# Performance work log

Hardware: AMD Instinct MI355X
Metric: run time of the kernel (lower is better)

Reference implementation:

```python
import jax, jax.numpy as jnp
import numpy as np

# Approximate EMD matching (Fan et al. approxmatch): 10 annealed soft-assignment
# rounds with levels -4^j for j = 7..-1 and level 0 for the final round.
_LEVELS = jnp.asarray([-(4.0 ** j) for j in range(7, -2, -1)] + [0.0], dtype=jnp.float32)


def _approx_match(d2, n, m):
    # d2: [b, n, m] squared pairwise distances
    b = d2.shape[0]
    factorl = max(n, m) / float(n)
    factorr = max(n, m) / float(m)
    remainl0 = jnp.full((b, n), factorl, dtype=d2.dtype)
    remainr0 = jnp.full((b, m), factorr, dtype=d2.dtype)
    match0 = jnp.zeros_like(d2)

    def step(carry, level):
        match, remainl, remainr = carry
        w = jnp.exp(level * d2) * remainr[:, None, :]            # [b,n,m]
        w = w / (jnp.sum(w, axis=-1, keepdims=True) + 1e-9)      # row-normalize
        w = w * remainl[:, :, None]                              # scale by left capacity
        ss2 = jnp.sum(w, axis=1)                                 # [b,m] column mass
        s = jnp.minimum(remainr / (ss2 + 1e-9), 1.0)             # column saturation
        w = w * s[:, None, :]
        match = match + w
        remainl = jnp.maximum(remainl - jnp.sum(w, axis=-1), 0.0)
        remainr = jnp.maximum(remainr - jnp.sum(w, axis=1), 0.0)
        return (match, remainl, remainr), None

    (match, _, _), _ = jax.lax.scan(step, (match0, remainl0, remainr0), _LEVELS)
    return match


def setup_inputs() -> dict:
    key = jax.random.key(0)
    k1, k2 = jax.random.split(key)
    xyz1 = jax.random.normal(k1, (16, 2048, 3), dtype=jnp.float32)
    xyz2 = jax.random.normal(k2, (16, 2048, 3), dtype=jnp.float32)
    return {"xyz1": xyz1, "xyz2": xyz2}


def reference(xyz1, xyz2):
    n, m = xyz1.shape[1], xyz2.shape[1]
    diff = xyz1[:, :, None, :] - xyz2[:, None, :, :]             # [b,n,m,3]
    d2 = jnp.sum(diff * diff, axis=-1)                           # [b,n,m]
    match = _approx_match(d2, n, m)
    dist = jnp.sqrt(jnp.maximum(d2, 1e-12))
    cost = jnp.sum(match * dist, axis=(1, 2))                    # [b]
    return cost
```

## Files before the change

### kernel.cpp

```cpp
#include <hip/hip_runtime.h>
#include <math.h>

#define B 16
#define N 2048
#define M 2048
#define BN (B * N)
#define LOG2E 1.4426950408889634f

#define CJ 128
#define NCH (M / CJ)
#define TPB 128
#define RPT 4
#define RBLK (TPB * RPT)

#define EXP2F(x) __builtin_amdgcn_exp2f(x)
#define SQRTF(x) __builtin_amdgcn_sqrtf(x)

__global__ __launch_bounds__(1024) void k_sort(const float* __restrict__ xyz1,
                                               const float* __restrict__ xyz2,
                                               float4* __restrict__ p1,
                                               float4* __restrict__ p2,
                                               float2* __restrict__ ib,
                                               float2* __restrict__ jb) {
    __shared__ float key[2048];
    __shared__ int sidx[2048];
    const int wg = blockIdx.x;
    const int b = wg & (B - 1);
    const bool second = wg >= B;
    const float* src = second ? xyz2 : xyz1;
    const int tx = threadIdx.x;

    for (int t = tx; t < 2048; t += 1024) {
        key[t] = src[3 * (size_t)(b * 2048 + t)];
        sidx[t] = t;
    }
    __syncthreads();

    for (int k = 2; k <= 2048; k <<= 1) {
        for (int j = k >> 1; j > 0; j >>= 1) {
            int e = 2 * tx - (tx & (j - 1));
            int f = e + j;
            bool asc = ((e & k) == 0);
            float ke = key[e], kf = key[f];
            if ((ke > kf) == asc) {
                int ie = sidx[e], if_ = sidx[f];
                key[e] = kf;
                key[f] = ke;
                sidx[e] = if_;
                sidx[f] = ie;
            }
            __syncthreads();
        }
    }

    float4* dst = second ? p2 : p1;
    for (int t = tx; t < 2048; t += 1024) {
        int o = sidx[t];
        const float* s = src + 3 * (size_t)(b * 2048 + o);
        float x = s[0], y = s[1], z = s[2];
        dst[b * 2048 + t] = make_float4(x, y, z, fmaf(x, x, fmaf(y, y, z * z)));
    }
    if (tx < NCH) {
        float2 bb = make_float2(key[tx * CJ], key[tx * CJ + CJ - 1]);
        (second ? jb : ib)[b * NCH + tx] = bb;
    }
}

__global__ __launch_bounds__(256) void k_init(float* __restrict__ rl0,
                                              float* __restrict__ rr0,
                                              float* __restrict__ rs0,
                                              float* __restrict__ rs2,
                                              float* __restrict__ t1b,
                                              float* __restrict__ ss20,
                                              float* __restrict__ cost) {
    int idx = blockIdx.x * 256 + threadIdx.x;
    rl0[idx] = 1.0f;
    rr0[idx] = 1.0f;
    rs0[idx] = 0.0f;
    rs2[idx] = 0.0f;
    t1b[idx] = 0.0f;
    ss20[idx] = 0.0f;
    if (idx < B) cost[idx] = 0.0f;
}

__global__ __launch_bounds__(TPB, 2) void k_rowsum0(const float4* __restrict__ p1,
                                                    const float4* __restrict__ p2,
                                                    const float2* __restrict__ jb,
                                                    float* __restrict__ rs,
                                                    float c2, float sqD) {
    __shared__ float4 tile4[CJ];
    const int b = blockIdx.z;
    const int tx = threadIdx.x;
    const int i0 = blockIdx.y * RBLK + 4 * tx;

    {
        int gj = b * M + blockIdx.x * CJ + tx;
        float4 f = p2[gj];
        tile4[tx] = make_float4(f.x, f.y, f.z, c2 * f.w);
    }
    __syncthreads();

    float4 f0 = p1[b * N + i0];
    float4 f1 = p1[b * N + i0 + 1];
    float4 f2 = p1[b * N + i0 + 2];
    float4 f3 = p1[b * N + i0 + 3];
    float2 bnd = jb[b * NCH + blockIdx.x];
    bool skip = (bnd.x - f3.x > sqD) || (f0.x - bnd.y > sqD);

    float a0 = 0.0f, a1 = 0.0f, a2 = 0.0f, a3 = 0.0f;
    if (!skip) {
        const float m2c = -2.0f * c2;
        float X0 = m2c * f0.x, Y0 = m2c * f0.y, Z0 = m2c * f0.z, n0 = c2 * f0.w;
        float X1 = m2c * f1.x, Y1 = m2c * f1.y, Z1 = m2c * f1.z, n1 = c2 * f1.w;
        float X2 = m2c * f2.x, Y2 = m2c * f2.y, Z2 = m2c * f2.z, n2 = c2 * f2.w;
        float X3 = m2c * f3.x, Y3 = m2c * f3.y, Z3 = m2c * f3.z, n3 = c2 * f3.w;
#pragma unroll 8
        for (int t = 0; t < CJ; ++t) {
            float4 q4 = tile4[t];
            a0 += EXP2F(fmaf(q4.x, X0, fmaf(q4.y, Y0, fmaf(q4.z, Z0, n0 + q4.w))));
            a1 += EXP2F(fmaf(q4.x, X1, fmaf(q4.y, Y1, fmaf(q4.z, Z1, n1 + q4.w))));
            a2 += EXP2F(fmaf(q4.x, X2, fmaf(q4.y, Y2, fmaf(q4.z, Z2, n2 + q4.w))));
            a3 += EXP2F(fmaf(q4.x, X3, fmaf(q4.y, Y3, fmaf(q4.z, Z3, n3 + q4.w))));
        }
    }
    atomicAdd(&rs[b * N + i0], a0);
    atomicAdd(&rs[b * N + i0 + 1], a1);
    atomicAdd(&rs[b * N + i0 + 2], a2);
    atomicAdd(&rs[b * N + i0 + 3], a3);
}

__global__ __launch_bounds__(TPB, 2) void k_colsum(const float4* __restrict__ p1,
                                                   const float4* __restrict__ p2,
                                                   const float2* __restrict__ ib,
                                                   const float* __restrict__ rl_in,
                                                   float* __restrict__ rl_out,
                                                   const float* __restrict__ rs_prev,
                                                   const float* __restrict__ rs_cur,
                                                   float* __restrict__ rs_zero,
                                                   const float* __restrict__ t1_in,
                                                   float* __restrict__ t1_zero,
                                                   const float* __restrict__ rr,
                                                   float* __restrict__ ss2_acc,
                                                   float cS, float sqD) {
    __shared__ float4 tile4[CJ];
    __shared__ float tileA[CJ];
    const int b = blockIdx.z;
    const int tx = threadIdx.x;
    const int j0 = blockIdx.y * RBLK + 4 * tx;

    {
        int gi = b * N + blockIdx.x * CJ + tx;
        float4 f = p1[gi];
        float rlo = rl_in[gi];
        float ap = rlo / (rs_prev[gi] + 1e-9f);
        float rln = fmaxf(rlo - ap * t1_in[gi], 0.0f);
        float a = rln / (rs_cur[gi] + 1e-9f);
        tile4[tx] = make_float4(f.x, f.y, f.z, cS * f.w);
        tileA[tx] = a;
        if (blockIdx.y == 0) {
            rl_out[gi] = rln;
            t1_zero[gi] = 0.0f;
            rs_zero[gi] = 0.0f;
        }
    }
    __syncthreads();

    float4 f0 = p2[b * M + j0];
    float4 f1 = p2[b * M + j0 + 1];
    float4 f2 = p2[b * M + j0 + 2];
    float4 f3 = p2[b * M + j0 + 3];
    float2 bnd = ib[b * NCH + blockIdx.x];
    bool skip = (bnd.x - f3.x > sqD) || (f0.x - bnd.y > sqD);

    float a0 = 0.0f, a1 = 0.0f, a2 = 0.0f, a3 = 0.0f;
    if (!skip) {
        const float m2c = -2.0f * cS;
        float X0 = m2c * f0.x, Y0 = m2c * f0.y, Z0 = m2c * f0.z, n0 = cS * f0.w;
        float X1 = m2c * f1.x, Y1 = m2c * f1.y, Z1 = m2c * f1.z, n1 = cS * f1.w;
        float X2 = m2c * f2.x, Y2 = m2c * f2.y, Z2 = m2c * f2.z, n2 = cS * f2.w;
        float X3 = m2c * f3.x, Y3 = m2c * f3.y, Z3 = m2c * f3.z, n3 = cS * f3.w;
#pragma unroll 8
        for (int t = 0; t < CJ; ++t) {
            float4 q4 = tile4[t];
            float av = tileA[t];
            a0 = fmaf(EXP2F(fmaf(q4.x, X0, fmaf(q4.y, Y0, fmaf(q4.z, Z0, n0 + q4.w)))), av, a0);
            a1 = fmaf(EXP2F(fmaf(q4.x, X1, fmaf(q4.y, Y1, fmaf(q4.z, Z1, n1 + q4.w)))), av, a1);
            a2 = fmaf(EXP2F(fmaf(q4.x, X2, fmaf(q4.y, Y2, fmaf(q4.z, Z2, n2 + q4.w)))), av, a2);
            a3 = fmaf(EXP2F(fmaf(q4.x, X3, fmaf(q4.y, Y3, fmaf(q4.z, Z3, n3 + q4.w)))), av, a3);
        }
    }
    atomicAdd(&ss2_acc[b * M + j0], a0 * rr[b * M + j0]);
    atomicAdd(&ss2_acc[b * M + j0 + 1], a1 * rr[b * M + j0 + 1]);
    atomicAdd(&ss2_acc[b * M + j0 + 2], a2 * rr[b * M + j0 + 2]);
    atomicAdd(&ss2_acc[b * M + j0 + 3], a3 * rr[b * M + j0 + 3]);
}

__global__ __launch_bounds__(256) void k_suma(const float* __restrict__ rl_in,
                                              float* __restrict__ rl_out,
                                              const float* __restrict__ rs_prev,
                                              const float* __restrict__ rs_cur,
                                              const float* __restrict__ t1_in,
                                              float* __restrict__ S) {
    __shared__ float red[4];
    const int b = blockIdx.x;
    const int tx = threadIdx.x;
    float s = 0.0f;
#pragma unroll
    for (int k = 0; k < N / 256; ++k) {
        int gi = b * N + k * 256 + tx;
        float rlo = rl_in[gi];
        float ap = rlo / (rs_prev[gi] + 1e-9f);
        float rln = fmaxf(rlo - ap * t1_in[gi], 0.0f);
        rl_out[gi] = rln;
        s += rln / (rs_cur[gi] + 1e-9f);
    }
#pragma unroll
    for (int off = 32; off > 0; off >>= 1)
        s += __shfl_down(s, off, 64);
    if ((tx & 63) == 0) red[tx >> 6] = s;
    __syncthreads();
    if (tx == 0) S[b] = red[0] + red[1] + red[2] + red[3];
}

__global__ __launch_bounds__(256) void k_mulss2(const float* __restrict__ rr,
                                                const float* __restrict__ S,
                                                float* __restrict__ ss2_out) {
    int idx = blockIdx.x * 256 + threadIdx.x;
    ss2_out[idx] = rr[idx] * S[idx >> 11];
}

template <int MODE>
__global__ __launch_bounds__(TPB, 2) void k_fused(const float4* __restrict__ p1,
                                                  const float4* __restrict__ p2,
                                                  const float2* __restrict__ jb,
                                                  const float* __restrict__ rr_in,
                                                  float* __restrict__ rr_out,
                                                  const float* __restrict__ ss2_in,
                                                  float* __restrict__ ss2_zero,
                                                  const float* __restrict__ rl_new,
                                                  const float* __restrict__ rs_cur,
                                                  float* __restrict__ rs_next,
                                                  float* __restrict__ t1_acc,
                                                  float* __restrict__ cost,
                                                  float cS, float rsq, float sqD) {
    __shared__ float4 tile4[CJ];
    __shared__ float2 tile2[CJ];
    const int b = blockIdx.z;
    const int tx = threadIdx.x;
    const int i0 = blockIdx.y * RBLK + 4 * tx;

    {
        int gj = b * M + blockIdx.x * CJ + tx;
        float4 f = p2[gj];
        float rrv = rr_in[gj];
        float sv = ss2_in[gj];
        float s = fminf(rrv / (sv + 1e-9f), 1.0f);
        float q = rrv * s;
        float rrn = fmaxf(rrv - sv * s, 0.0f);
        tile4[tx] = make_float4(f.x, f.y, f.z, q);
        tile2[tx] = make_float2(rrn, cS * f.w);
        if (MODE != 2 && blockIdx.y == 0) {
            rr_out[gj] = rrn;
            ss2_zero[gj] = 0.0f;
        }
    }
    __syncthreads();

    float4 f0 = p1[b * N + i0];
    float4 f1 = p1[b * N + i0 + 1];
    float4 f2 = p1[b * N + i0 + 2];
    float4 f3 = p1[b * N + i0 + 3];
    float2 bnd = jb[b * NCH + blockIdx.x];
    bool skip = (MODE == 0) && ((bnd.x - f3.x > sqD) || (f0.x - bnd.y > sqD));

    float T10 = 0.0f, T11 = 0.0f, T12 = 0.0f, T13 = 0.0f;
    float T20 = 0.0f, T21 = 0.0f, T22 = 0.0f, T23 = 0.0f;
    float rs0 = 0.0f, rs1 = 0.0f, rs2v = 0.0f, rs3 = 0.0f;
    if (!skip) {
        const float m2c = -2.0f * cS;
        float X0 = m2c * f0.x, Y0 = m2c * f0.y, Z0 = m2c * f0.z, n0 = cS * f0.w;
        float X1 = m2c * f1.x, Y1 = m2c * f1.y, Z1 = m2c * f1.z, n1 = cS * f1.w;
        float X2 = m2c * f2.x, Y2 = m2c * f2.y, Z2 = m2c * f2.z, n2 = cS * f2.w;
        float X3 = m2c * f3.x, Y3 = m2c * f3.y, Z3 = m2c * f3.z, n3 = cS * f3.w;
#pragma unroll 8
        for (int t = 0; t < CJ; ++t) {
            float4 q4 = tile4[t];
            float2 rn = tile2[t];
            float g0 = fmaf(q4.x, X0, fmaf(q4.y, Y0, fmaf(q4.z, Z0, n0 + rn.y)));
            float g1 = fmaf(q4.x, X1, fmaf(q4.y, Y1, fmaf(q4.z, Z1, n1 + rn.y)));
            float g2 = fmaf(q4.x, X2, fmaf(q4.y, Y2, fmaf(q4.z, Z2, n2 + rn.y)));
            float g3 = fmaf(q4.x, X3, fmaf(q4.y, Y3, fmaf(q4.z, Z3, n3 + rn.y)));
            float sd0 = SQRTF(fabsf(g0)), sd1 = SQRTF(fabsf(g1));
            float sd2 = SQRTF(fabsf(g2)), sd3 = SQRTF(fabsf(g3));
            float w0, w1, w2, w3;
            if (MODE == 0) {
                float e0 = EXP2F(g0), e1 = EXP2F(g1), e2 = EXP2F(g2), e3 = EXP2F(g3);
                float s0 = e0 * e0, s1 = e1 * e1, s2 = e2 * e2, s3 = e3 * e3;
                w0 = (s0 * s0) * q4.w;
                w1 = (s1 * s1) * q4.w;
                w2 = (s2 * s2) * q4.w;
                w3 = (s3 * s3) * q4.w;
                rs0 = fmaf(e0, rn.x, rs0);
                rs1 = fmaf(e1, rn.x, rs1);
                rs2v = fmaf(e2, rn.x, rs2v);
                rs3 = fmaf(e3, rn.x, rs3);
            } else if (MODE == 1) {
                w0 = EXP2F(g0) * q4.w;
                w1 = EXP2F(g1) * q4.w;
                w2 = EXP2F(g2) * q4.w;
                w3 = EXP2F(g3) * q4.w;
                rs0 += rn.x;
                rs1 += rn.x;
                rs2v += rn.x;
                rs3 += rn.x;
            } else {
                w0 = q4.w;
                w1 = q4.w;
                w2 = q4.w;
                w3 = q4.w;
            }
            T10 += w0;
            T11 += w1;
            T12 += w2;
            T13 += w3;
            T20 = fmaf(w0, sd0, T20);
            T21 = fmaf(w1, sd1, T21);
            T22 = fmaf(w2, sd2, T22);
            T23 = fmaf(w3, sd3, T23);
        }
    }

    const int gi0 = b * N + i0;
    if (MODE != 2) {
        atomicAdd(&t1_acc[gi0], T10);
        atomicAdd(&t1_acc[gi0 + 1], T11);
        atomicAdd(&t1_acc[gi0 + 2], T12);
        atomicAdd(&t1_acc[gi0 + 3], T13);
        atomicAdd(&rs_next[gi0], rs0);
        atomicAdd(&rs_next[gi0 + 1], rs1);
        atomicAdd(&rs_next[gi0 + 2], rs2v);
        atomicAdd(&rs_next[gi0 + 3], rs3);
    }

    float aa = rl_new[gi0] / (rs_cur[gi0] + 1e-9f);
    float ab = rl_new[gi0 + 1] / (rs_cur[gi0 + 1] + 1e-9f);
    float ac = rl_new[gi0 + 2] / (rs_cur[gi0 + 2] + 1e-9f);
    float ad = rl_new[gi0 + 3] / (rs_cur[gi0 + 3] + 1e-9f);
    float contrib = rsq * fmaf(aa, T20, fmaf(ab, T21, fmaf(ac, T22, ad * T23)));
#pragma unroll
    for (int off = 32; off > 0; off >>= 1)
        contrib += __shfl_down(contrib, off, 64);
    if ((tx & 63) == 0) atomicAdd(&cost[b], contrib);
}

extern "C" void kernel_launch(void* const* d_in, const int* in_sizes, int n_in,
                              void* d_out, int out_size, void* d_ws, size_t ws_size,
                              hipStream_t stream) {
    const float* xyz1 = (const float*)d_in[0];
    const float* xyz2 = (const float*)d_in[1];
    float* cost = (float*)d_out;

    float* ws = (float*)d_ws;
    float* rl[2] = {ws + 0 * BN, ws + 1 * BN};
    float* rr[2] = {ws + 2 * BN, ws + 3 * BN};
    float* rs[3] = {ws + 4 * BN, ws + 5 * BN, ws + 6 * BN};
    float* ss2b[2] = {ws + 7 * BN, ws + 8 * BN};
    float* t1[2] = {ws + 9 * BN, ws + 10 * BN};
    float4* p1 = (float4*)(ws + 11 * BN);
    float4* p2 = (float4*)(ws + 15 * BN);
    float* S = ws + 19 * BN;
    float2* ib = (float2*)(ws + 19 * BN + 64);
    float2* jb = (float2*)(ws + 19 * BN + 64 + 512);

    static const float levels[10] = {-16384.0f, -4096.0f, -1024.0f, -256.0f,
                                     -64.0f,    -16.0f,   -4.0f,    -1.0f,
                                     -0.25f,    0.0f};
    float c2[10], sqD[10];
    for (int l = 0; l < 10; ++l) {
        c2[l] = levels[l] * LOG2E;
        sqD[l] = (l < 9) ? sqrtf(150.0f / fabsf(c2[l])) : 1e30f;
    }

    dim3 grid(NCH, N / RBLK, B);
    dim3 blk(TPB);
    dim3 gs(BN / 256);
    dim3 b256(256);

    k_sort<<<dim3(2 * B), dim3(1024), 0, stream>>>(xyz1, xyz2, p1, p2, ib, jb);
    k_init<<<gs, b256, 0, stream>>>(rl[0], rr[0], rs[0], rs[2], t1[1], ss2b[0], cost);
    k_rowsum0<<<grid, blk, 0, stream>>>(p1, p2, jb, rs[0], c2[0], sqD[0]);

    for (int l = 0; l < 10; ++l) {
        int p = l & 1;
        if (l < 9) {
            k_colsum<<<grid, blk, 0, stream>>>(
                p1, p2, ib, rl[p], rl[1 - p], rs[(l + 2) % 3], rs[l % 3],
                rs[(l + 1) % 3], t1[1 - p], t1[p], rr[p], ss2b[p], c2[l], sqD[l]);
        } else {
            k_suma<<<dim3(B), b256, 0, stream>>>(
                rl[p], rl[1 - p], rs[(l + 2) % 3], rs[l % 3], t1[1 - p], S);
            k_mulss2<<<gs, b256, 0, stream>>>(rr[p], S, ss2b[p]);
        }

        if (l <= 7) {
            float cS = c2[l + 1];
            float rsq = 1.0f / sqrtf(fabsf(cS));
            k_fused<0><<<grid, blk, 0, stream>>>(
                p1, p2, jb, rr[p], rr[1 - p], ss2b[p], ss2b[1 - p], rl[1 - p],
                rs[l % 3], rs[(l + 1) % 3], t1[p], cost, cS, rsq, sqD[l + 1]);
        } else if (l == 8) {
            float cS = c2[8];
            float rsq = 1.0f / sqrtf(fabsf(cS));
            k_fused<1><<<grid, blk, 0, stream>>>(
                p1, p2, jb, rr[p], rr[1 - p], ss2b[p], ss2b[1 - p], rl[1 - p],
                rs[l % 3], rs[(l + 1) % 3], t1[p], cost, cS, rsq, 1e30f);
        } else {
            k_fused<2><<<grid, blk, 0, stream>>>(
                p1, p2, jb, rr[p], rr[1 - p], ss2b[p], ss2b[1 - p], rl[1 - p],
                rs[l % 3], rs[(l + 1) % 3], t1[p], cost, 1.0f, 1.0f, 1e30f);
        }
    }
}
```

Baseline: 669.7 us.

## Shrink blocks to one wavefront and skip whole tiles via block-level bounds

Halves the threads per block to a single 64-lane wavefront and switches each thread's four rows from a contiguous stride to a TPB stride, so global loads and atomics are coalesced. The distance-based culling test moves from a per-thread check to a per-block early return using the first and last sorted x of the block's range. Whole wavefronts can then exit before doing any exp work. The risk is more, smaller blocks, looped tile loads, and a coarser cull that may skip fewer tiles.

```diff
diff --git a/kernel.cpp b/kernel.cpp
--- a/kernel.cpp
+++ b/kernel.cpp
@@ -9,7 +9,7 @@
 
 #define CJ 128
 #define NCH (M / CJ)
-#define TPB 128
+#define TPB 64
 #define RPT 4
 #define RBLK (TPB * RPT)
 
@@ -91,42 +91,44 @@
     __shared__ float4 tile4[CJ];
     const int b = blockIdx.z;
     const int tx = threadIdx.x;
-    const int i0 = blockIdx.y * RBLK + 4 * tx;
-
-    {
-        int gj = b * M + blockIdx.x * CJ + tx;
+    const int base = blockIdx.y * RBLK;
+    const int i0 = base + tx;
+
+    for (int t = tx; t < CJ; t += TPB) {
+        int gj = b * M + blockIdx.x * CJ + t;
         float4 f = p2[gj];
-        tile4[tx] = make_float4(f.x, f.y, f.z, c2 * f.w);
+        tile4[t] = make_float4(f.x, f.y, f.z, c2 * f.w);
     }
     __syncthreads();
 
+    float2 bnd = jb[b * NCH + blockIdx.x];
+    float rlo = p1[b * N + base].x;
+    float rhi = p1[b * N + base + RBLK - 1].x;
+    if ((bnd.x - rhi > sqD) || (rlo - bnd.y > sqD)) return;
+
     float4 f0 = p1[b * N + i0];
-    float4 f1 = p1[b * N + i0 + 1];
-    float4 f2 = p1[b * N + i0 + 2];
-    float4 f3 = p1[b * N + i0 + 3];
-    float2 bnd = jb[b * NCH + blockIdx.x];
-    bool skip = (bnd.x - f3.x > sqD) || (f0.x - bnd.y > sqD);
+    float4 f1 = p1[b * N + i0 + TPB];
+    float4 f2 = p1[b * N + i0 + 2 * TPB];
+    float4 f3 = p1[b * N + i0 + 3 * TPB];
+    const float m2c = -2.0f * c2;
+    float X0 = m2c * f0.x, Y0 = m2c * f0.y, Z0 = m2c * f0.z, n0 = c2 * f0.w;
+    float X1 = m2c * f1.x, Y1 = m2c * f1.y, Z1 = m2c * f1.z, n1 = c2 * f1.w;
+    float X2 = m2c * f2.x, Y2 = m2c * f2.y, Z2 = m2c * f2.z, n2 = c2 * f2.w;
+    float X3 = m2c * f3.x, Y3 = m2c * f3.y, Z3 = m2c * f3.z, n3 = c2 * f3.w;
 
     float a0 = 0.0f, a1 = 0.0f, a2 = 0.0f, a3 = 0.0f;
-    if (!skip) {
-        const float m2c = -2.0f * c2;
-        float X0 = m2c * f0.x, Y0 = m2c * f0.y, Z0 = m2c * f0.z, n0 = c2 * f0.w;
-        float X1 = m2c * f1.x, Y1 = m2c * f1.y, Z1 = m2c * f1.z, n1 = c2 * f1.w;
-        float X2 = m2c * f2.x, Y2 = m2c * f2.y, Z2 = m2c * f2.z, n2 = c2 * f2.w;
-        float X3 = m2c * f3.x, Y3 = m2c * f3.y, Z3 = m2c * f3.z, n3 = c2 * f3.w;
 #pragma unroll 8
-        for (int t = 0; t < CJ; ++t) {
-            float4 q4 = tile4[t];
-            a0 += EXP2F(fmaf(q4.x, X0, fmaf(q4.y, Y0, fmaf(q4.z, Z0, n0 + q4.w))));
-            a1 += EXP2F(fmaf(q4.x, X1, fmaf(q4.y, Y1, fmaf(q4.z, Z1, n1 + q4.w))));
-            a2 += EXP2F(fmaf(q4.x, X2, fmaf(q4.y, Y2, fmaf(q4.z, Z2, n2 + q4.w))));
-            a3 += EXP2F(fmaf(q4.x, X3, fmaf(q4.y, Y3, fmaf(q4.z, Z3, n3 + q4.w))));
-        }
+    for (int t = 0; t < CJ; ++t) {
+        float4 q4 = tile4[t];
+        a0 += EXP2F(fmaf(q4.x, X0, fmaf(q4.y, Y0, fmaf(q4.z, Z0, n0 + q4.w))));
+        a1 += EXP2F(fmaf(q4.x, X1, fmaf(q4.y, Y1, fmaf(q4.z, Z1, n1 + q4.w))));
+        a2 += EXP2F(fmaf(q4.x, X2, fmaf(q4.y, Y2, fmaf(q4.z, Z2, n2 + q4.w))));
+        a3 += EXP2F(fmaf(q4.x, X3, fmaf(q4.y, Y3, fmaf(q4.z, Z3, n3 + q4.w))));
     }
     atomicAdd(&rs[b * N + i0], a0);
-    atomicAdd(&rs[b * N + i0 + 1], a1);
-    atomicAdd(&rs[b * N + i0 + 2], a2);
-    atomicAdd(&rs[b * N + i0 + 3], a3);
+    atomicAdd(&rs[b * N + i0 + TPB], a1);
+    atomicAdd(&rs[b * N + i0 + 2 * TPB], a2);
+    atomicAdd(&rs[b * N + i0 + 3 * TPB], a3);
 }
 
 __global__ __launch_bounds__(TPB, 2) void k_colsum(const float4* __restrict__ p1,
@@ -146,17 +148,18 @@
     __shared__ float tileA[CJ];
     const int b = blockIdx.z;
     const int tx = threadIdx.x;
-    const int j0 = blockIdx.y * RBLK + 4 * tx;
-
-    {
-        int gi = b * N + blockIdx.x * CJ + tx;
+    const int base = blockIdx.y * RBLK;
+    const int j0 = base + tx;
+
+    for (int t = tx; t < CJ; t += TPB) {
+        int gi = b * N + blockIdx.x * CJ + t;
         float4 f = p1[gi];
         float rlo = rl_in[gi];
         float ap = rlo / (rs_prev[gi] + 1e-9f);
         float rln = fmaxf(rlo - ap * t1_in[gi], 0.0f);
         float a = rln / (rs_cur[gi] + 1e-9f);
-        tile4[tx] = make_float4(f.x, f.y, f.z, cS * f.w);
-        tileA[tx] = a;
+        tile4[t] = make_float4(f.x, f.y, f.z, cS * f.w);
+        tileA[t] = a;
         if (blockIdx.y == 0) {
             rl_out[gi] = rln;
             t1_zero[gi] = 0.0f;
@@ -165,34 +168,35 @@
     }
     __syncthreads();
 
+    float2 bnd = ib[b * NCH + blockIdx.x];
+    float clo = p2[b * M + base].x;
+    float chi = p2[b * M + base + RBLK - 1].x;
+    if ((bnd.x - chi > sqD) || (clo - bnd.y > sqD)) return;
+
     float4 f0 = p2[b * M + j0];
-    float4 f1 = p2[b * M + j0 + 1];
-    float4 f2 = p2[b * M + j0 + 2];
-    float4 f3 = p2[b * M + j0 + 3];
-    float2 bnd = ib[b * NCH + blockIdx.x];
-    bool skip = (bnd.x - f3.x > sqD) || (f0.x - bnd.y > sqD);
+    float4 f1 = p2[b * M + j0 + TPB];
+    float4 f2 = p2[b * M + j0 + 2 * TPB];
+    float4 f3 = p2[b * M + j0 + 3 * TPB];
+    const float m2c = -2.0f * cS;
+    float X0 = m2c * f0.x, Y0 = m2c * f0.y, Z0 = m2c * f0.z, n0 = cS * f0.w;
+    float X1 = m2c * f1.x, Y1 = m2c * f1.y, Z1 = m2c * f1.z, n1 = cS * f1.w;
+    float X2 = m2c * f2.x, Y2 = m2c * f2.y, Z2 = m2c * f2.z, n2 = cS * f2.w;
+    float X3 = m2c * f3.x, Y3 = m2c * f3.y, Z3 = m2c * f3.z, n3 = cS * f3.w;
 
     float a0 = 0.0f, a1 = 0.0f, a2 = 0.0f, a3 = 0.0f;
-    if (!skip) {
-        const float m2c = -2.0f * cS;
-        float X0 = m2c * f0.x, Y0 = m2c * f0.y, Z0 = m2c * f0.z, n0 = cS * f0.w;
-        float X1 = m2c * f1.x, Y1 = m2c * f1.y, Z1 = m2c * f1.z, n1 = cS * f1.w;
-        float X2 = m2c * f2.x, Y2 = m2c * f2.y, Z2 = m2c * f2.z, n2 = cS * f2.w;
-        float X3 = m2c * f3.x, Y3 = m2c * f3.y, Z3 = m2c * f3.z, n3 = cS * f3.w;
 #pragma unroll 8
-        for (int t = 0; t < CJ; ++t) {
-            float4 q4 = tile4[t];
-            float av = tileA[t];
-            a0 = fmaf(EXP2F(fmaf(q4.x, X0, fmaf(q4.y, Y0, fmaf(q4.z, Z0, n0 + q4.w)))), av, a0);
-            a1 = fmaf(EXP2F(fmaf(q4.x, X1, fmaf(q4.y, Y1, fmaf(q4.z, Z1, n1 + q4.w)))), av, a1);
-            a2 = fmaf(EXP2F(fmaf(q4.x, X2, fmaf(q4.y, Y2, fmaf(q4.z, Z2, n2 + q4.w)))), av, a2);
-            a3 = fmaf(EXP2F(fmaf(q4.x, X3, fmaf(q4.y, Y3, fmaf(q4.z, Z3, n3 + q4.w)))), av, a3);
-        }
+    for (int t = 0; t < CJ; ++t) {
+        float4 q4 = tile4[t];
+        float av = tileA[t];
+        a0 = fmaf(EXP2F(fmaf(q4.x, X0, fmaf(q4.y, Y0, fmaf(q4.z, Z0, n0 + q4.w)))), av, a0);
+        a1 = fmaf(EXP2F(fmaf(q4.x, X1, fmaf(q4.y, Y1, fmaf(q4.z, Z1, n1 + q4.w)))), av, a1);
+        a2 = fmaf(EXP2F(fmaf(q4.x, X2, fmaf(q4.y, Y2, fmaf(q4.z, Z2, n2 + q4.w)))), av, a2);
+        a3 = fmaf(EXP2F(fmaf(q4.x, X3, fmaf(q4.y, Y3, fmaf(q4.z, Z3, n3 + q4.w)))), av, a3);
     }
     atomicAdd(&ss2_acc[b * M + j0], a0 * rr[b * M + j0]);
-    atomicAdd(&ss2_acc[b * M + j0 + 1], a1 * rr[b * M + j0 + 1]);
-    atomicAdd(&ss2_acc[b * M + j0 + 2], a2 * rr[b * M + j0 + 2]);
-    atomicAdd(&ss2_acc[b * M + j0 + 3], a3 * rr[b * M + j0 + 3]);
+    atomicAdd(&ss2_acc[b * M + j0 + TPB], a1 * rr[b * M + j0 + TPB]);
+    atomicAdd(&ss2_acc[b * M + j0 + 2 * TPB], a2 * rr[b * M + j0 + 2 * TPB]);
+    atomicAdd(&ss2_acc[b * M + j0 + 3 * TPB], a3 * rr[b * M + j0 + 3 * TPB]);
 }
 
 __global__ __launch_bounds__(256) void k_suma(const float* __restrict__ rl_in,
@@ -247,18 +251,19 @@
     __shared__ float2 tile2[CJ];
     const int b = blockIdx.z;
     const int tx = threadIdx.x;
-    const int i0 = blockIdx.y * RBLK + 4 * tx;
-
-    {
-        int gj = b * M + blockIdx.x * CJ + tx;
+    const int base = blockIdx.y * RBLK;
+    const int i0 = base + tx;
+
+    for (int t = tx; t < CJ; t += TPB) {
+        int gj = b * M + blockIdx.x * CJ + t;
         float4 f = p2[gj];
         float rrv = rr_in[gj];
         float sv = ss2_in[gj];
         float s = fminf(rrv / (sv + 1e-9f), 1.0f);
         float q = rrv * s;
         float rrn = fmaxf(rrv - sv * s, 0.0f);
-        tile4[tx] = make_float4(f.x, f.y, f.z, q);
-        tile2[tx] = make_float2(rrn, cS * f.w);
+        tile4[t] = make_float4(f.x, f.y, f.z, q);
+        tile2[t] = make_float2(rrn, cS * f.w);
         if (MODE != 2 && blockIdx.y == 0) {
             rr_out[gj] = rrn;
             ss2_zero[gj] = 0.0f;
@@ -266,91 +271,94 @@
     }
     __syncthreads();
 
+    if (MODE == 0) {
+        float2 bnd = jb[b * NCH + blockIdx.x];
+        float rlo = p1[b * N + base].x;
+        float rhi = p1[b * N + base + RBLK - 1].x;
+        if ((bnd.x - rhi > sqD) || (rlo - bnd.y > sqD)) return;
+    }
+
     float4 f0 = p1[b * N + i0];
-    float4 f1 = p1[b * N + i0 + 1];
-    float4 f2 = p1[b * N + i0 + 2];
-    float4 f3 = p1[b * N + i0 + 3];
-    float2 bnd = jb[b * NCH + blockIdx.x];
-    bool skip = (MODE == 0) && ((bnd.x - f3.x > sqD) || (f0.x - bnd.y > sqD));
+    float4 f1 = p1[b * N + i0 + TPB];
+    float4 f2 = p1[b * N + i0 + 2 * TPB];
+    float4 f3 = p1[b * N + i0 + 3 * TPB];
+    const float m2c = -2.0f * cS;
+    float X0 = m2c * f0.x, Y0 = m2c * f0.y, Z0 = m2c * f0.z, n0 = cS * f0.w;
+    float X1 = m2c * f1.x, Y1 = m2c * f1.y, Z1 = m2c * f1.z, n1 = cS * f1.w;
+    float X2 = m2c * f2.x, Y2 = m2c * f2.y, Z2 = m2c * f2.z, n2 = cS * f2.w;
+    float X3 = m2c * f3.x, Y3 = m2c * f3.y, Z3 = m2c * f3.z, n3 = cS * f3.w;
 
     float T10 = 0.0f, T11 = 0.0f, T12 = 0.0f, T13 = 0.0f;
     float T20 = 0.0f, T21 = 0.0f, T22 = 0.0f, T23 = 0.0f;
     float rs0 = 0.0f, rs1 = 0.0f, rs2v = 0.0f, rs3 = 0.0f;
-    if (!skip) {
-        const float m2c = -2.0f * cS;
-        float X0 = m2c * f0.x, Y0 = m2c * f0.y, Z0 = m2c * f0.z, n0 = cS * f0.w;
-        float X1 = m2c * f1.x, Y1 = m2c * f1.y, Z1 = m2c * f1.z, n1 = cS * f1.w;
-        float X2 = m2c * f2.x, Y2 = m2c * f2.y, Z2 = m2c * f2.z, n2 = cS * f2.w;
-        float X3 = m2c * f3.x, Y3 = m2c * f3.y, Z3 = m2c * f3.z, n3 = cS * f3.w;
 #pragma unroll 8
-        for (int t = 0; t < CJ; ++t) {
-            float4 q4 = tile4[t];
-            float2 rn = tile2[t];
-            float g0 = fmaf(q4.x, X0, fmaf(q4.y, Y0, fmaf(q4.z, Z0, n0 + rn.y)));
-            float g1 = fmaf(q4.x, X1, fmaf(q4.y, Y1, fmaf(q4.z, Z1, n1 + rn.y)));
-            float g2 = fmaf(q4.x, X2, fmaf(q4.y, Y2, fmaf(q4.z, Z2, n2 + rn.y)));
-            float g3 = fmaf(q4.x, X3, fmaf(q4.y, Y3, fmaf(q4.z, Z3, n3 + rn.y)));
-            float sd0 = SQRTF(fabsf(g0)), sd1 = SQRTF(fabsf(g1));
-            float sd2 = SQRTF(fabsf(g2)), sd3 = SQRTF(fabsf(g3));
-            float w0, w1, w2, w3;
-            if (MODE == 0) {
-                float e0 = EXP2F(g0), e1 = EXP2F(g1), e2 = EXP2F(g2), e3 = EXP2F(g3);
-                float s0 = e0 * e0, s1 = e1 * e1, s2 = e2 * e2, s3 = e3 * e3;
-                w0 = (s0 * s0) * q4.w;
-                w1 = (s1 * s1) * q4.w;
-                w2 = (s2 * s2) * q4.w;
-                w3 = (s3 * s3) * q4.w;
-                rs0 = fmaf(e0, rn.x, rs0);
-                rs1 = fmaf(e1, rn.x, rs1);
-                rs2v = fmaf(e2, rn.x, rs2v);
-                rs3 = fmaf(e3, rn.x, rs3);
-            } else if (MODE == 1) {
-                w0 = EXP2F(g0) * q4.w;
-                w1 = EXP2F(g1) * q4.w;
-                w2 = EXP2F(g2) * q4.w;
-                w3 = EXP2F(g3) * q4.w;
-                rs0 += rn.x;
-                rs1 += rn.x;
-                rs2v += rn.x;
-                rs3 += rn.x;
-            } else {
-                w0 = q4.w;
-                w1 = q4.w;
-                w2 = q4.w;
-                w3 = q4.w;
-            }
-            T10 += w0;
-            T11 += w1;
-            T12 += w2;
-            T13 += w3;
-            T20 = fmaf(w0, sd0, T20);
-            T21 = fmaf(w1, sd1, T21);
-            T22 = fmaf(w2, sd2, T22);
-            T23 = fmaf(w3, sd3, T23);
-        }
+    for (int t = 0; t < CJ; ++t) {
+        float4 q4 = tile4[t];
+        float2 rn = tile2[t];
+        float g0 = fmaf(q4.x, X0, fmaf(q4.y, Y0, fmaf(q4.z, Z0, n0 + rn.y)));
+        float g1 = fmaf(q4.x, X1, fmaf(q4.y, Y1, fmaf(q4.z, Z1, n1 + rn.y)));
+        float g2 = fmaf(q4.x, X2, fmaf(q4.y, Y2, fmaf(q4.z, Z2, n2 + rn.y)));
+        float g3 = fmaf(q4.x, X3, fmaf(q4.y, Y3, fmaf(q4.z, Z3, n3 + rn.y)));
+        float sd0 = SQRTF(fabsf(g0)), sd1 = SQRTF(fabsf(g1));
+        float sd2 = SQRTF(fabsf(g2)), sd3 = SQRTF(fabsf(g3));
+        float w0, w1, w2, w3;
+        if (MODE == 0) {
+            float e0 = EXP2F(g0), e1 = EXP2F(g1), e2 = EXP2F(g2), e3 = EXP2F(g3);
+            float s0 = e0 * e0, s1 = e1 * e1, s2 = e2 * e2, s3 = e3 * e3;
+            w0 = (s0 * s0) * q4.w;
+            w1 = (s1 * s1) * q4.w;
+            w2 = (s2 * s2) * q4.w;
+            w3 = (s3 * s3) * q4.w;
+            rs0 = fmaf(e0, rn.x, rs0);
+            rs1 = fmaf(e1, rn.x, rs1);
+            rs2v = fmaf(e2, rn.x, rs2v);
+            rs3 = fmaf(e3, rn.x, rs3);
+        } else if (MODE == 1) {
+            w0 = EXP2F(g0) * q4.w;
+            w1 = EXP2F(g1) * q4.w;
+            w2 = EXP2F(g2) * q4.w;
+            w3 = EXP2F(g3) * q4.w;
+            rs0 += rn.x;
+            rs1 += rn.x;
+            rs2v += rn.x;
+            rs3 += rn.x;
+        } else {
+            w0 = q4.w;
+            w1 = q4.w;
+            w2 = q4.w;
+            w3 = q4.w;
+        }
+        T10 += w0;
+        T11 += w1;
+        T12 += w2;
+        T13 += w3;
+        T20 = fmaf(w0, sd0, T20);
+        T21 = fmaf(w1, sd1, T21);
+        T22 = fmaf(w2, sd2, T22);
+        T23 = fmaf(w3, sd3, T23);
     }
 
     const int gi0 = b * N + i0;
     if (MODE != 2) {
         atomicAdd(&t1_acc[gi0], T10);
-        atomicAdd(&t1_acc[gi0 + 1], T11);
-        atomicAdd(&t1_acc[gi0 + 2], T12);
-        atomicAdd(&t1_acc[gi0 + 3], T13);
+        atomicAdd(&t1_acc[gi0 + TPB], T11);
+        atomicAdd(&t1_acc[gi0 + 2 * TPB], T12);
+        atomicAdd(&t1_acc[gi0 + 3 * TPB], T13);
         atomicAdd(&rs_next[gi0], rs0);
-        atomicAdd(&rs_next[gi0 + 1], rs1);
-        atomicAdd(&rs_next[gi0 + 2], rs2v);
-        atomicAdd(&rs_next[gi0 + 3], rs3);
+        atomicAdd(&rs_next[gi0 + TPB], rs1);
+        atomicAdd(&rs_next[gi0 + 2 * TPB], rs2v);
+        atomicAdd(&rs_next[gi0 + 3 * TPB], rs3);
     }
 
     float aa = rl_new[gi0] / (rs_cur[gi0] + 1e-9f);
-    float ab = rl_new[gi0 + 1] / (rs_cur[gi0 + 1] + 1e-9f);
-    float ac = rl_new[gi0 + 2] / (rs_cur[gi0 + 2] + 1e-9f);
-    float ad = rl_new[gi0 + 3] / (rs_cur[gi0 + 3] + 1e-9f);
+    float ab = rl_new[gi0 + TPB] / (rs_cur[gi0 + TPB] + 1e-9f);
+    float ac = rl_new[gi0 + 2 * TPB] / (rs_cur[gi0 + 2 * TPB] + 1e-9f);
+    float ad = rl_new[gi0 + 3 * TPB] / (rs_cur[gi0 + 3 * TPB] + 1e-9f);
     float contrib = rsq * fmaf(aa, T20, fmaf(ab, T21, fmaf(ac, T22, ad * T23)));
 #pragma unroll
     for (int off = 32; off > 0; off >>= 1)
         contrib += __shfl_down(contrib, off, 64);
-    if ((tx & 63) == 0) atomicAdd(&cost[b], contrib);
+    if (tx == 0) atomicAdd(&cost[b], contrib);
 }
 
 extern "C" void kernel_launch(void* const* d_in, const int* in_sizes, int n_in,
```

New measurement: 616.1 us. 1.09x faster.
